# Kernel optimization log

Measured on AMD Instinct MI355X. Metric: run time of the kernel, lower is better.

## Reference

```python
import jax, jax.numpy as jnp
import numpy as np

ALPHA = 2.0
K_HOPS = 3
N_NODES, N_EDGES, IN_DIM = 8192, 131072, 128


def _mlp(coeffs, W0, W1, W2, W3):
    # MLP(n_layers=n_hidden_layers+2=4, relu between, no bias, bn/dropout off in eval)
    h = jax.nn.relu(coeffs @ W0)
    h = jax.nn.relu(h @ W1)
    h = jax.nn.relu(h @ W2)
    return h @ W3  # [N, 1] rotation angles


def _aggregate_k_hop(edge_index, angles):
    # Faithful translation of aggregate_k_hop including its in-place aliasing:
    # enhanced_angles aliases angles, and step_k ACCUMULATES across hops
    # (torch_scatter reduces into the provided out tensor).
    N = angles.shape[0]
    row, col = edge_index[0], edge_index[1]
    f = lambda k: jnp.exp(jnp.asarray(-ALPHA * k, angles.dtype))
    # hop 1: scatter-add over the raw edge list (duplicate edges counted, as in original)
    step = jax.ops.segment_sum(angles[col] * f(1), row, num_segments=N)
    enhanced = angles + step
    # Dense boolean adjacency: composing paths then np.unique(axis=1) is exactly the
    # 'exists a k-step walk' indicator, i.e. boolean adjacency powers.
    adj = jnp.zeros((N, N), jnp.float32).at[row, col].set(1.0)
    P = adj
    for k in range(2, K_HOPS + 1):
        P = ((P @ adj) > 0).astype(jnp.float32)  # unique k-walk pairs
        step = step + f(k) * (P @ enhanced)      # reads angles AFTER previous in-place add
        enhanced = enhanced + step               # step accumulates across hops
    return enhanced


def setup_inputs() -> dict:
    key = jax.random.key(0)
    k0, k1, k2, k3, k4, k5 = jax.random.split(key, 6)
    s = 1.0 / np.sqrt(IN_DIM)
    return {
        "coeffs": jax.random.normal(k0, (N_NODES, IN_DIM), jnp.float32),
        "W0": jax.random.normal(k1, (IN_DIM, IN_DIM), jnp.float32) * s,
        "W1": jax.random.normal(k2, (IN_DIM, IN_DIM), jnp.float32) * s,
        "W2": jax.random.normal(k3, (IN_DIM, IN_DIM), jnp.float32) * s,
        "W3": jax.random.normal(k4, (IN_DIM, 1), jnp.float32) * s,
        "edge_index": jax.random.randint(k5, (2, N_EDGES), 0, N_NODES, dtype=jnp.int32),
    }


def reference(coeffs, W0, W1, W2, W3, edge_index):
    angles = _mlp(coeffs, W0, W1, W2, W3)
    return _aggregate_k_hop(edge_index, angles)  # batch.node_rotation_angles, [N, 1]
```

## Files before the change

kernel.cpp:

```cpp
#include <hip/hip_runtime.h>

constexpr int N    = 8192;
constexpr int NE   = 131072;
constexpr int WPR  = N / 32;
constexpr int MAXD = 64;

#define F1 0.13533528323661270f
#define F2 0.018315638888734179f
#define F3 0.0024787521766663585f

using bf16x8 = __attribute__((ext_vector_type(8))) short;
using f32x4  = __attribute__((ext_vector_type(4))) float;

__device__ __forceinline__ unsigned short f2bf(float f) {
    unsigned int u = __float_as_uint(f);
    u = (u + 0x7FFFu + ((u >> 16) & 1u)) >> 16;
    return (unsigned short)u;
}

__global__ __launch_bounds__(256) void prelude(
    const float* __restrict__ W0, const float* __restrict__ W1,
    const float* __restrict__ W2, unsigned short* __restrict__ Wt_g,
    uint4* __restrict__ zbase)
{
    int gt = blockIdx.x * 256 + threadIdx.x;
    if (gt < 4096) zbase[gt] = (uint4){0u, 0u, 0u, 0u};

    int l = gt >> 14;
    int r = gt & 16383;
    int k = r >> 7;
    int n = r & 127;
    const float* W = (l == 0) ? W0 : (l == 1) ? W1 : W2;
    Wt_g[l * 16384 + n * 128 + k] = f2bf(W[k * 128 + n]);
}

__global__ __launch_bounds__(256) void mlp_kernel(
    const float* __restrict__ X, const unsigned short* __restrict__ Wt_g,
    const float* __restrict__ W3, float* __restrict__ angles)
{
    __shared__ unsigned short Xb[32 * 136];
    __shared__ unsigned short Wt[128 * 136];
    __shared__ float part[2][32];

    const int tid  = threadIdx.x;
    const int row0 = blockIdx.x * 32;
    const int w  = tid >> 6, l = tid & 63;
    const int mt = w & 1, nh = w >> 1;
    const int lm = l & 15, lq = l >> 4;

    for (int q = tid; q < 32 * 32; q += 256) {
        float4 v = *(const float4*)&X[row0 * 128 + q * 4];
        ushort4 b;
        b.x = f2bf(v.x); b.y = f2bf(v.y); b.z = f2bf(v.z); b.w = f2bf(v.w);
        *(ushort4*)&Xb[(q >> 5) * 136 + (q & 31) * 4] = b;
    }

    for (int layer = 0; layer < 3; ++layer) {
        const unsigned short* Wg = Wt_g + layer * 16384;
        for (int q = tid; q < 2048; q += 256) {
            int n = q >> 4, ck = (q & 15) * 8;
            uint4 v = *(const uint4*)&Wg[n * 128 + ck];
            *(uint4*)&Wt[n * 136 + ck] = v;
        }
        __syncthreads();

        f32x4 acc[4];
#pragma unroll
        for (int t = 0; t < 4; ++t) acc[t] = (f32x4){0.f, 0.f, 0.f, 0.f};

#pragma unroll
        for (int kc = 0; kc < 4; ++kc) {
            bf16x8 a = *(const bf16x8*)&Xb[(mt * 16 + lm) * 136 + kc * 32 + lq * 8];
#pragma unroll
            for (int t = 0; t < 4; ++t) {
                bf16x8 b = *(const bf16x8*)
                    &Wt[(nh * 64 + t * 16 + lm) * 136 + kc * 32 + lq * 8];
                acc[t] = __builtin_amdgcn_mfma_f32_16x16x32_bf16(a, b, acc[t], 0, 0, 0);
            }
        }

#pragma unroll
        for (int t = 0; t < 4; ++t)
#pragma unroll
            for (int r = 0; r < 4; ++r) acc[t][r] = fmaxf(acc[t][r], 0.0f);

        __syncthreads();

        if (layer < 2) {
#pragma unroll
            for (int t = 0; t < 4; ++t)
#pragma unroll
                for (int r = 0; r < 4; ++r)
                    Xb[(mt * 16 + lq * 4 + r) * 136 + nh * 64 + t * 16 + lm] =
                        f2bf(acc[t][r]);
        } else {
            float p[4] = {0.f, 0.f, 0.f, 0.f};
#pragma unroll
            for (int t = 0; t < 4; ++t) {
                float w3v = W3[nh * 64 + t * 16 + lm];
#pragma unroll
                for (int r = 0; r < 4; ++r) p[r] += acc[t][r] * w3v;
            }
#pragma unroll
            for (int r = 0; r < 4; ++r) {
                p[r] += __shfl_xor(p[r], 1, 64);
                p[r] += __shfl_xor(p[r], 2, 64);
                p[r] += __shfl_xor(p[r], 4, 64);
                p[r] += __shfl_xor(p[r], 8, 64);
            }
            if (lm == 0)
#pragma unroll
                for (int r = 0; r < 4; ++r)
                    part[nh][mt * 16 + lq * 4 + r] = p[r];
            __syncthreads();
            if (tid < 32) angles[row0 + tid] = part[0][tid] + part[1][tid];
        }
    }
}

__global__ void edges_kernel(const int* __restrict__ ei,
                             const float* __restrict__ angles,
                             float* __restrict__ s1,
                             int* __restrict__ cnt_g,
                             int* __restrict__ nbr_g)
{
    int e = blockIdx.x * blockDim.x + threadIdx.x;
    if (e < NE) {
        int r = ei[e];
        int c = ei[NE + e];
        int p = atomicAdd(&cnt_g[r], 1);
        if (p < MAXD) nbr_g[r * MAXD + p] = c;
        atomicAdd(&s1[r], F1 * angles[c]);
    }
}

__global__ __launch_bounds__(256) void p2_kernel(
    const int* __restrict__ cnt_g, const int* __restrict__ nbr_g,
    unsigned int* __restrict__ P2,
    const float* __restrict__ angles, const float* __restrict__ s1,
    float* __restrict__ s2, float* __restrict__ e2)
{
    __shared__ unsigned int bm[4][WPR];
    __shared__ int nbr[4][MAXD];
    __shared__ int nc[4][MAXD];

    const int wv = threadIdx.x >> 6;
    const int l  = threadIdx.x & 63;
    const int i  = blockIdx.x * 4 + wv;

#pragma unroll
    for (int s = 0; s < 4; ++s) bm[wv][s * 64 + l] = 0u;

    const int n = min(cnt_g[i], MAXD);
    if (l < n) {
        int m = nbr_g[i * MAXD + l];
        nbr[wv][l] = m;
        nc[wv][l]  = min(cnt_g[m], MAXD);
    }
    __syncthreads();

    for (int q = 0; q < n; ++q) {
        int m  = nbr[wv][q];
        int c2 = nc[wv][q];
        if (l < c2) {
            int id = nbr_g[m * MAXD + l];
            atomicOr(&bm[wv][id >> 5], 1u << (id & 31));
        }
    }
    __syncthreads();

    unsigned int w[4];
#pragma unroll
    for (int s = 0; s < 4; ++s) {
        w[s] = bm[wv][s * 64 + l];
        P2[(size_t)i * WPR + s * 64 + l] = w[s];
    }

    float local = 0.0f;
#pragma unroll
    for (int s = 0; s < 4; ++s) {
        unsigned int ww = w[s];
        const int base = (s * 64 + l) * 32;
        while (ww) {
            int b = __ffs(ww) - 1;
            ww &= ww - 1;
            local += angles[base + b] + s1[base + b];
        }
    }
#pragma unroll
    for (int m = 1; m < 64; m <<= 1) local += __shfl_xor(local, m, 64);
    if (l == 0) {
        float e1i = angles[i] + s1[i];
        float s2v = s1[i] + F2 * local;
        s2[i] = s2v;
        e2[i] = e1i + s2v;
    }
}

__global__ __launch_bounds__(256) void p3_kernel(
    const unsigned int* __restrict__ P2,
    const int* __restrict__ cnt_g, const int* __restrict__ nbr_g,
    const float* __restrict__ e2, const float* __restrict__ s2,
    float* __restrict__ out)
{
    __shared__ int nbr[4][MAXD];

    const int wv = threadIdx.x >> 6;
    const int l  = threadIdx.x & 63;
    const int i  = blockIdx.x * 4 + wv;

    const int n = min(cnt_g[i], MAXD);
    if (l < n) nbr[wv][l] = nbr_g[i * MAXD + l];
    __syncthreads();

    unsigned int w[4] = {0u, 0u, 0u, 0u};
    for (int q = 0; q < n; ++q) {
        const unsigned int* rowp = P2 + (size_t)nbr[wv][q] * WPR + l;
#pragma unroll
        for (int s = 0; s < 4; ++s) w[s] |= rowp[s * 64];
    }

    float local = 0.0f;
#pragma unroll
    for (int c = 0; c < 32; ++c) {
        unsigned int wd  = __shfl(w[c >> 3], ((c & 7) << 3) | (l >> 3), 64);
        unsigned int nib = wd >> ((l & 7) * 4);
        float4 v = *(const float4*)&e2[c * 256 + l * 4];
        local += (nib & 1u) ? v.x : 0.0f;
        local += (nib & 2u) ? v.y : 0.0f;
        local += (nib & 4u) ? v.z : 0.0f;
        local += (nib & 8u) ? v.w : 0.0f;
    }
#pragma unroll
    for (int m = 1; m < 64; m <<= 1) local += __shfl_xor(local, m, 64);
    if (l == 0)
        out[i] = e2[i] + s2[i] + F3 * local;
}

extern "C" void kernel_launch(void* const* d_in, const int* in_sizes, int n_in,
                              void* d_out, int out_size, void* d_ws, size_t ws_size,
                              hipStream_t stream)
{
    const float* coeffs = (const float*)d_in[0];
    const float* W0     = (const float*)d_in[1];
    const float* W1     = (const float*)d_in[2];
    const float* W2     = (const float*)d_in[3];
    const float* W3     = (const float*)d_in[4];
    const int*   ei     = (const int*)  d_in[5];
    float* out = (float*)d_out;

    char* ws = (char*)d_ws;
    float*          angles = (float*)(ws + 0 * 32768);
    float*          s2     = (float*)(ws + 1 * 32768);
    float*          e2     = (float*)(ws + 2 * 32768);
    unsigned short* Wt_g   = (unsigned short*)(ws + 4 * 32768);
    int*            nbr_g  = (int*)  (ws + (1u  << 20));
    float*          s1     = (float*)(ws + (4u  << 20));
    int*            cnt_g  = (int*)  (ws + (4u  << 20) + 32768);
    unsigned int*   P2     = (unsigned int*)(ws + (5u  << 20));

    prelude<<<192, 256, 0, stream>>>(W0, W1, W2, Wt_g, (uint4*)s1);

    mlp_kernel<<<N / 32, 256, 0, stream>>>(coeffs, Wt_g, W3, angles);

    edges_kernel<<<NE / 256, 256, 0, stream>>>(ei, angles, s1, cnt_g, nbr_g);
    p2_kernel<<<N / 4, 256, 0, stream>>>(cnt_g, nbr_g, P2, angles, s1, s2, e2);
    p3_kernel<<<N / 4, 256, 0, stream>>>(P2, cnt_g, nbr_g, e2, s2, out);
}
```

Measured before the change: 127.0 us.

## Fuse weight prelude into MLP, parallelize P2 neighbor loop, stage e2 in LDS

Removes the separate prelude kernel: each MLP block now transposes and converts its own fp32 weights to bf16 and zeroes its slice of s1/cnt. p2 processes four neighbors per iteration using 16-lane subgroups instead of one neighbor per wave iteration. p3 uses 512-thread blocks and caches the full e2 vector in shared memory before the masked reduction. The changes trade redundant per-block weight conversion and a 32KB LDS copy per p3 block for one fewer launch and better lane utilization.

```diff
diff --git a/kernel.cpp b/kernel.cpp
--- a/kernel.cpp
+++ b/kernel.cpp
@@ -18,25 +18,11 @@
     return (unsigned short)u;
 }
 
-__global__ __launch_bounds__(256) void prelude(
+__global__ __launch_bounds__(256) void mlp_kernel(
+    const float* __restrict__ X,
     const float* __restrict__ W0, const float* __restrict__ W1,
-    const float* __restrict__ W2, unsigned short* __restrict__ Wt_g,
-    uint4* __restrict__ zbase)
-{
-    int gt = blockIdx.x * 256 + threadIdx.x;
-    if (gt < 4096) zbase[gt] = (uint4){0u, 0u, 0u, 0u};
-
-    int l = gt >> 14;
-    int r = gt & 16383;
-    int k = r >> 7;
-    int n = r & 127;
-    const float* W = (l == 0) ? W0 : (l == 1) ? W1 : W2;
-    Wt_g[l * 16384 + n * 128 + k] = f2bf(W[k * 128 + n]);
-}
-
-__global__ __launch_bounds__(256) void mlp_kernel(
-    const float* __restrict__ X, const unsigned short* __restrict__ Wt_g,
-    const float* __restrict__ W3, float* __restrict__ angles)
+    const float* __restrict__ W2, const float* __restrict__ W3,
+    float* __restrict__ angles, uint4* __restrict__ zbase)
 {
     __shared__ unsigned short Xb[32 * 136];
     __shared__ unsigned short Wt[128 * 136];
@@ -48,6 +34,11 @@
     const int mt = w & 1, nh = w >> 1;
     const int lm = l & 15, lq = l >> 4;
 
+    if (tid < 16) {
+        uint4 z; z.x = z.y = z.z = z.w = 0u;
+        zbase[blockIdx.x * 16 + tid] = z;
+    }
+
     for (int q = tid; q < 32 * 32; q += 256) {
         float4 v = *(const float4*)&X[row0 * 128 + q * 4];
         ushort4 b;
@@ -56,11 +47,17 @@
     }
 
     for (int layer = 0; layer < 3; ++layer) {
-        const unsigned short* Wg = Wt_g + layer * 16384;
-        for (int q = tid; q < 2048; q += 256) {
-            int n = q >> 4, ck = (q & 15) * 8;
-            uint4 v = *(const uint4*)&Wg[n * 128 + ck];
-            *(uint4*)&Wt[n * 136 + ck] = v;
+        const float* __restrict__ W = (layer == 0) ? W0 : (layer == 1) ? W1 : W2;
+        for (int it = 0; it < 16; ++it) {
+            int flat = it * 256 + tid;
+            int n  = flat & 127;
+            int k0 = (flat >> 7) << 2;
+            ushort4 b;
+            b.x = f2bf(W[(k0 + 0) * 128 + n]);
+            b.y = f2bf(W[(k0 + 1) * 128 + n]);
+            b.z = f2bf(W[(k0 + 2) * 128 + n]);
+            b.w = f2bf(W[(k0 + 3) * 128 + n]);
+            *(ushort4*)&Wt[n * 136 + k0] = b;
         }
         __syncthreads();
 
@@ -144,9 +141,11 @@
     __shared__ int nbr[4][MAXD];
     __shared__ int nc[4][MAXD];
 
-    const int wv = threadIdx.x >> 6;
-    const int l  = threadIdx.x & 63;
-    const int i  = blockIdx.x * 4 + wv;
+    const int wv  = threadIdx.x >> 6;
+    const int l   = threadIdx.x & 63;
+    const int i   = blockIdx.x * 4 + wv;
+    const int qq  = l >> 4;
+    const int sub = l & 15;
 
 #pragma unroll
     for (int s = 0; s < 4; ++s) bm[wv][s * 64 + l] = 0u;
@@ -159,11 +158,12 @@
     }
     __syncthreads();
 
-    for (int q = 0; q < n; ++q) {
-        int m  = nbr[wv][q];
-        int c2 = nc[wv][q];
-        if (l < c2) {
-            int id = nbr_g[m * MAXD + l];
+    for (int q0 = 0; q0 < n; q0 += 4) {
+        int q = q0 + qq;
+        int m = 0, c2 = 0;
+        if (q < n) { m = nbr[wv][q]; c2 = nc[wv][q]; }
+        for (int s = sub; s < c2; s += 16) {
+            int id = nbr_g[m * MAXD + s];
             atomicOr(&bm[wv][id >> 5], 1u << (id & 31));
         }
     }
@@ -197,17 +197,22 @@
     }
 }
 
-__global__ __launch_bounds__(256) void p3_kernel(
+__global__ __launch_bounds__(512) void p3_kernel(
     const unsigned int* __restrict__ P2,
     const int* __restrict__ cnt_g, const int* __restrict__ nbr_g,
     const float* __restrict__ e2, const float* __restrict__ s2,
     float* __restrict__ out)
 {
-    __shared__ int nbr[4][MAXD];
-
-    const int wv = threadIdx.x >> 6;
-    const int l  = threadIdx.x & 63;
-    const int i  = blockIdx.x * 4 + wv;
+    __shared__ float e2s[N];
+    __shared__ int nbr[8][MAXD];
+
+    const int tid = threadIdx.x;
+    const int wv  = tid >> 6;
+    const int l   = tid & 63;
+    const int i   = blockIdx.x * 8 + wv;
+
+    for (int q = tid; q < N / 4; q += 512)
+        *(float4*)&e2s[q * 4] = *(const float4*)&e2[q * 4];
 
     const int n = min(cnt_g[i], MAXD);
     if (l < n) nbr[wv][l] = nbr_g[i * MAXD + l];
@@ -225,7 +230,7 @@
     for (int c = 0; c < 32; ++c) {
         unsigned int wd  = __shfl(w[c >> 3], ((c & 7) << 3) | (l >> 3), 64);
         unsigned int nib = wd >> ((l & 7) * 4);
-        float4 v = *(const float4*)&e2[c * 256 + l * 4];
+        float4 v = *(const float4*)&e2s[c * 256 + l * 4];
         local += (nib & 1u) ? v.x : 0.0f;
         local += (nib & 2u) ? v.y : 0.0f;
         local += (nib & 4u) ? v.z : 0.0f;
@@ -253,17 +258,15 @@
     float*          angles = (float*)(ws + 0 * 32768);
     float*          s2     = (float*)(ws + 1 * 32768);
     float*          e2     = (float*)(ws + 2 * 32768);
-    unsigned short* Wt_g   = (unsigned short*)(ws + 4 * 32768);
     int*            nbr_g  = (int*)  (ws + (1u  << 20));
     float*          s1     = (float*)(ws + (4u  << 20));
     int*            cnt_g  = (int*)  (ws + (4u  << 20) + 32768);
     unsigned int*   P2     = (unsigned int*)(ws + (5u  << 20));
 
-    prelude<<<192, 256, 0, stream>>>(W0, W1, W2, Wt_g, (uint4*)s1);
-
-    mlp_kernel<<<N / 32, 256, 0, stream>>>(coeffs, Wt_g, W3, angles);
+    mlp_kernel<<<N / 32, 256, 0, stream>>>(coeffs, W0, W1, W2, W3, angles,
+                                           (uint4*)s1);
 
     edges_kernel<<<NE / 256, 256, 0, stream>>>(ei, angles, s1, cnt_g, nbr_g);
     p2_kernel<<<N / 4, 256, 0, stream>>>(cnt_g, nbr_g, P2, angles, s1, s2, e2);
-    p3_kernel<<<N / 4, 256, 0, stream>>>(P2, cnt_g, nbr_g, e2, s2, out);
-}
+    p3_kernel<<<N / 8, 512, 0, stream>>>(P2, cnt_g, nbr_g, e2, s2, out);
+}
```

New measurement: 120.4 us. -5.2%, faster.
